# Kernel tuning notes

Measured on AMD Instinct MI355X. Metric: run time of the kernel, lower is better.

The kernel has to match this reference:

```python
import jax, jax.numpy as jnp
import numpy as np

N = 100000
E = 1600000

def gcn_conv(x, w, b, row, col, ew, n):
    # PyG GCNConv: linear transform, add self-loops (weight 1), symmetric
    # degree normalization with edge weights, scatter-sum to destinations.
    h = x @ w  # [N, out]
    loop = jnp.arange(n)
    row2 = jnp.concatenate([row, loop])
    col2 = jnp.concatenate([col, loop])
    ew2 = jnp.concatenate([ew, jnp.ones((n,), x.dtype)])
    deg = jax.ops.segment_sum(ew2, col2, num_segments=n)
    dinv = jnp.where(deg > 0, jax.lax.rsqrt(deg), jnp.zeros_like(deg))
    norm = dinv[row2] * ew2 * dinv[col2]  # [E+N]
    msg = h[row2] * norm[:, None]  # [E+N, out]
    out = jax.ops.segment_sum(msg, col2, num_segments=n)
    return out + b


def setup_inputs() -> dict:
    key = jax.random.key(0)
    ks = jax.random.split(key, 8)
    x = jax.random.normal(ks[0], (N, 256), dtype=jnp.float32)
    edge_index = jax.random.randint(ks[1], (2, E), 0, N, dtype=jnp.int64)
    edge_attr = jax.random.uniform(ks[2], (E,), dtype=jnp.float32)
    w_dense = jax.random.normal(ks[3], (256, 256), dtype=jnp.float32) * 0.05
    b_dense = jnp.zeros((256,), jnp.float32)
    w_enc = jax.random.normal(ks[4], (256, 256), dtype=jnp.float32) * 0.05
    b_enc = jnp.zeros((256,), jnp.float32)
    w_mu = jax.random.normal(ks[5], (256, 128), dtype=jnp.float32) * 0.05
    b_mu = jnp.zeros((128,), jnp.float32)
    w_logstd = jax.random.normal(ks[6], (256, 128), dtype=jnp.float32) * 0.05
    b_logstd = jnp.zeros((128,), jnp.float32)
    return {"x": x, "edge_index": edge_index, "edge_attr": edge_attr,
            "w_dense": w_dense, "b_dense": b_dense, "w_enc": w_enc, "b_enc": b_enc,
            "w_mu": w_mu, "b_mu": b_mu, "w_logstd": w_logstd, "b_logstd": b_logstd}


def reference(x, edge_index, edge_attr, w_dense, b_dense, w_enc, b_enc, w_mu, b_mu, w_logstd, b_logstd):
    row, col = edge_index[0], edge_index[1]
    h = jax.nn.relu(x @ w_dense + b_dense)  # dense + relu; dropout is identity in eval
    # enc_layer=2 -> encoder[:-1] applies exactly one hidden GCNConv
    h = gcn_conv(h, w_enc, b_enc, row, col, edge_attr, N)
    mu = gcn_conv(h, w_mu, b_mu, row, col, edge_attr, N)
    logstd = gcn_conv(h, w_logstd, b_logstd, row, col, edge_attr, N)
    return (mu, logstd)
```

## Files before the change

### kernel.cpp

```cpp
#include <hip/hip_runtime.h>


typedef short bf16x8 __attribute__((ext_vector_type(8)));
typedef float f32x4 __attribute__((ext_vector_type(4)));

static __device__ __forceinline__ unsigned int f2bf(float f) {
    unsigned int u = __float_as_uint(f);
    return ((u + 0x7fffu + ((u >> 16) & 1u)) >> 16) & 0xffffu;
}
static __device__ __forceinline__ float bf2f(unsigned int us) {
    return __uint_as_float(us << 16);
}

static __device__ __forceinline__ void load_lds16(const void* g, void* l) {
    __builtin_amdgcn_global_load_lds(
        (const __attribute__((address_space(1))) unsigned int*)g,
        (__attribute__((address_space(3))) unsigned int*)l, 16, 0, 0);
}

#define FIXSCALE 8388608.0f


__global__ __launch_bounds__(256) void init_kernel(unsigned long long* acc, int n) {
    int i = blockIdx.x * 256 + threadIdx.x;
    if (i < n) acc[i] = 0ull;
}

__global__ __launch_bounds__(256) void edge_pack_kernel(const int* __restrict__ col,
                                                        const float* __restrict__ ew,
                                                        unsigned long long* __restrict__ acc,
                                                        unsigned int* __restrict__ rank, int E) {
    int e = blockIdx.x * 256 + threadIdx.x;
    if (e < E) {
        int c = col[e];
        unsigned long long pk = (1ull << 32) |
                                (unsigned long long)(unsigned int)(ew[e] * FIXSCALE + 0.5f);
        unsigned long long old = atomicAdd(&acc[c], pk);
        rank[e] = (unsigned int)(old >> 32);
    }
}

__global__ __launch_bounds__(256) void dinv_kernel(const unsigned long long* __restrict__ acc,
                                                   float* __restrict__ dinv, int n) {
    int i = blockIdx.x * 256 + threadIdx.x;
    if (i < n) {
        float deg = 1.0f + (float)(unsigned int)acc[i] * (1.0f / FIXSCALE);
        dinv[i] = rsqrtf(deg);
    }
}

__global__ __launch_bounds__(1024) void scanA_kernel(const unsigned long long* __restrict__ acc,
                                                     int* __restrict__ offsets,
                                                     int* __restrict__ bsum, int n) {
    __shared__ int wsum[16];
    int tid = threadIdx.x, lane = tid & 63, wv = tid >> 6;
    int i = blockIdx.x * 1024 + tid;
    int v = (i < n) ? (int)(acc[i] >> 32) : 0;
    int s = v;
#pragma unroll
    for (int off = 1; off < 64; off <<= 1) {
        int t = __shfl_up(s, off, 64);
        if (lane >= off) s += t;
    }
    if (lane == 63) wsum[wv] = s;
    __syncthreads();
    if (wv == 0 && lane < 16) {
        int w = wsum[lane];
        int ss = w;
#pragma unroll
        for (int off = 1; off < 16; off <<= 1) {
            int t = __shfl_up(ss, off, 64);
            if (lane >= off) ss += t;
        }
        wsum[lane] = ss - w;
        if (lane == 15) bsum[blockIdx.x] = ss;
    }
    __syncthreads();
    if (i < n) offsets[i] = wsum[wv] + s - v;
}

__global__ __launch_bounds__(128) void scanB_kernel(int* __restrict__ bsum, int nb,
                                                    int* __restrict__ offsets, int n) {
    __shared__ int w0tot;
    int tid = threadIdx.x, lane = tid & 63, wv = tid >> 6;
    int v = (tid < nb) ? bsum[tid] : 0;
    int s = v;
#pragma unroll
    for (int off = 1; off < 64; off <<= 1) {
        int t = __shfl_up(s, off, 64);
        if (lane >= off) s += t;
    }
    if (wv == 0 && lane == 63) w0tot = s;
    __syncthreads();
    int excl = s - v + (wv ? w0tot : 0);
    if (tid < nb) bsum[tid] = excl;
    if (tid == nb - 1) offsets[n] = excl + v;
}

__global__ __launch_bounds__(256) void scanC_kernel(int* __restrict__ offsets,
                                                    const int* __restrict__ bsum, int n) {
    int i = blockIdx.x * 256 + threadIdx.x;
    if (i < n) offsets[i] += bsum[i >> 10];
}

__global__ __launch_bounds__(256) void fill2_kernel(const int* __restrict__ row,
                                                    const int* __restrict__ col,
                                                    const float* __restrict__ ew,
                                                    const unsigned int* __restrict__ rank,
                                                    const int* __restrict__ offsets,
                                                    const float* __restrict__ dinv,
                                                    uint2* __restrict__ edges, int E) {
    int e = blockIdx.x * 256 + threadIdx.x;
    if (e < E) {
        int c = col[e];
        int r = row[e];
        int pos = offsets[c] + (int)rank[e];
        uint2 p;
        p.x = (unsigned int)r;
        p.y = __float_as_uint(dinv[r] * ew[e]);
        edges[pos] = p;
    }
}

__global__ __launch_bounds__(256) void cvt_frag_kernel(const float* __restrict__ x,
                                                       unsigned short* __restrict__ Af, int n) {
    int g = blockIdx.x * 256 + threadIdx.x;
    int c = g >> 6, lane = g & 63;
    if (c >= n) return;
    float4 v = ((const float4*)x)[(size_t)c * 64 + lane];
    uint2 w;
    w.x = f2bf(v.x) | (f2bf(v.y) << 16);
    w.y = f2bf(v.z) | (f2bf(v.w) << 16);
    int T = c >> 4, l = c & 15;
    size_t idx8 = (size_t)T * 1024 + (size_t)((lane >> 3)) * 128 + ((lane >> 1) & 3) * 32 + l * 2 + (lane & 1);
    ((uint2*)Af)[idx8] = w;
}

__global__ __launch_bounds__(256) void splitw_kernel(const float* __restrict__ W, int M,
                                                     unsigned short* __restrict__ hi,
                                                     unsigned short* __restrict__ lo) {
    int idx = blockIdx.x * 256 + threadIdx.x;
    if (idx < M * 256) {
        int c = idx >> 8, k = idx & 255;
        float w = W[k * M + c];
        unsigned int h = f2bf(w);
        float r = w - bf2f(h);
        int T = c >> 4, l = c & 15, K = k >> 5, q = (k >> 3) & 3, j = k & 7;
        size_t o = (size_t)(T * 8 + K) * 512 + q * 128 + l * 8 + j;
        hi[o] = (unsigned short)h;
        lo[o] = (unsigned short)f2bf(r);
    }
}

__global__ __launch_bounds__(256) void bcat_kernel(const float* __restrict__ a,
                                                   const float* __restrict__ b,
                                                   float* __restrict__ o) {
    int t = threadIdx.x;
    o[t] = (t < 128) ? a[t] : b[t - 128];
}

#define ACC8(qv, uv)                                      \
    do {                                                  \
        float w_ = __uint_as_float((qv).y);               \
        a0 += w_ * __uint_as_float((uv).x << 16);         \
        a1 += w_ * __uint_as_float((uv).x & 0xffff0000u); \
        a2 += w_ * __uint_as_float((uv).y << 16);         \
        a3 += w_ * __uint_as_float((uv).y & 0xffff0000u); \
        a4 += w_ * __uint_as_float((uv).z << 16);         \
        a5 += w_ * __uint_as_float((uv).z & 0xffff0000u); \
        a6 += w_ * __uint_as_float((uv).w << 16);         \
        a7 += w_ * __uint_as_float((uv).w & 0xffff0000u); \
    } while (0)

__global__ __launch_bounds__(256) void spmm_kernel(const unsigned short* __restrict__ h,
                                                   const uint2* __restrict__ edges,
                                                   const int* __restrict__ offsets,
                                                   const float* __restrict__ dinv,
                                                   unsigned short* __restrict__ outf, int n) {
    int wave = threadIdx.x >> 6;
    int lane = threadIdx.x & 63;
    int half = lane >> 5, hl = lane & 31;
    int c = blockIdx.x * 4 + wave;
    if (c >= n) return;
    const uint4* __restrict__ h4 = (const uint4*)h;
    float di = dinv[c];
    int beg = __builtin_amdgcn_readfirstlane(offsets[c]);
    int end = __builtin_amdgcn_readfirstlane(offsets[c + 1]);
    int d = end - beg;
    int elim = beg + (d & ~1);

    float a0 = 0.f, a1 = 0.f, a2 = 0.f, a3 = 0.f;
    float a4 = 0.f, a5 = 0.f, a6 = 0.f, a7 = 0.f;

    int e = beg;
    for (; e + 8 <= elim; e += 8) {
        uint2 q0 = edges[e + 0 + half];
        uint2 q1 = edges[e + 2 + half];
        uint2 q2 = edges[e + 4 + half];
        uint2 q3 = edges[e + 6 + half];
        uint4 u0 = h4[(size_t)q0.x * 32 + hl];
        uint4 u1 = h4[(size_t)q1.x * 32 + hl];
        uint4 u2 = h4[(size_t)q2.x * 32 + hl];
        uint4 u3 = h4[(size_t)q3.x * 32 + hl];
        ACC8(q0, u0);
        ACC8(q1, u1);
        ACC8(q2, u2);
        ACC8(q3, u3);
    }
    for (; e < elim; e += 2) {
        uint2 q = edges[e + half];
        uint4 u = h4[(size_t)q.x * 32 + hl];
        ACC8(q, u);
    }
    {
        uint2 qf;
        qf.x = (unsigned int)c;
        qf.y = half ? 0u : __float_as_uint(di);
        if (half && (d & 1)) qf = edges[end - 1];
        uint4 uf = h4[(size_t)qf.x * 32 + hl];
        ACC8(qf, uf);
    }

    a0 += __shfl_xor(a0, 32);
    a1 += __shfl_xor(a1, 32);
    a2 += __shfl_xor(a2, 32);
    a3 += __shfl_xor(a3, 32);
    a4 += __shfl_xor(a4, 32);
    a5 += __shfl_xor(a5, 32);
    a6 += __shfl_xor(a6, 32);
    a7 += __shfl_xor(a7, 32);

    if (half == 0) {
        uint4 wv;
        wv.x = f2bf(di * a0) | (f2bf(di * a1) << 16);
        wv.y = f2bf(di * a2) | (f2bf(di * a3) << 16);
        wv.z = f2bf(di * a4) | (f2bf(di * a5) << 16);
        wv.w = f2bf(di * a6) | (f2bf(di * a7) << 16);
        int T = c >> 4, l = c & 15;
        size_t o16 = ((size_t)T * 8 + (hl >> 2)) * 512 + (size_t)(hl & 3) * 128 + (size_t)l * 8;
        *(uint4*)(outf + o16) = wv;
    }
}

__global__ __launch_bounds__(256) void mfma_gemm_kernel(const unsigned short* __restrict__ Af,
                                                        const unsigned short* __restrict__ Wh,
                                                        const unsigned short* __restrict__ Wl,
                                                        const float* __restrict__ bias,
                                                        void* __restrict__ outp,
                                                        int n, int M, int flags) {
    __shared__ short lds[12288];
    int tid = threadIdx.x, lane = tid & 63, wave = tid >> 6;
    int wr = wave & 1, wc = wave >> 1;
    int l16 = lane & 15, quad = lane >> 4;
    int T0 = blockIdx.x * 8;
    int Tc0 = blockIdx.y * 8;

    f32x4 acc[4][4];
#pragma unroll
    for (int i = 0; i < 4; ++i)
#pragma unroll
        for (int j = 0; j < 4; ++j) acc[i][j] = (f32x4)0.0f;

    for (int K = 0; K < 8; ++K) {
#pragma unroll
        for (int j = 0; j < 6; ++j) {
            int cid = wave * 6 + j;
            const unsigned short* g;
            if (cid < 8)       g = Af + ((size_t)(T0 + cid) * 8 + K) * 512;
            else if (cid < 16) g = Wh + ((size_t)(Tc0 + cid - 8) * 8 + K) * 512;
            else               g = Wl + ((size_t)(Tc0 + cid - 16) * 8 + K) * 512;
            load_lds16(g + (size_t)lane * 8, lds + cid * 512);
        }
        __syncthreads();
        bf16x8 af[4], bh[4], bl[4];
#pragma unroll
        for (int t = 0; t < 4; ++t) {
            af[t] = *(const bf16x8*)(lds + (4 * wr + t) * 512 + lane * 8);
            bh[t] = *(const bf16x8*)(lds + 4096 + (4 * wc + t) * 512 + lane * 8);
            bl[t] = *(const bf16x8*)(lds + 8192 + (4 * wc + t) * 512 + lane * 8);
        }
#pragma unroll
        for (int rt = 0; rt < 4; ++rt)
#pragma unroll
            for (int ct = 0; ct < 4; ++ct) {
                acc[rt][ct] = __builtin_amdgcn_mfma_f32_16x16x32_bf16(af[rt], bh[ct], acc[rt][ct], 0, 0, 0);
                acc[rt][ct] = __builtin_amdgcn_mfma_f32_16x16x32_bf16(af[rt], bl[ct], acc[rt][ct], 0, 0, 0);
            }
        __syncthreads();
    }

    int relu = flags & 1, obf = flags & 2, dual = flags & 4;
    int r0 = T0 * 16, c0 = Tc0 * 16;
#pragma unroll
    for (int ct = 0; ct < 4; ++ct) {
        int col = c0 + 64 * wc + 16 * ct + l16;
        float b = bias[col];
#pragma unroll
        for (int rt = 0; rt < 4; ++rt) {
            int rbase = r0 + 64 * wr + 16 * rt + quad * 4;
#pragma unroll
            for (int i = 0; i < 4; ++i) {
                int r = rbase + i;
                if (r < n) {
                    float v = acc[rt][ct][i] + b;
                    if (relu) v = fmaxf(v, 0.0f);
                    if (dual)
                        ((float*)outp)[(size_t)(col >> 7) * ((size_t)n * 128) + (size_t)r * 128 + (col & 127)] = v;
                    else if (obf)
                        ((unsigned short*)outp)[(size_t)r * M + col] = (unsigned short)f2bf(v);
                    else
                        ((float*)outp)[(size_t)r * M + col] = v;
                }
            }
        }
    }
}


extern "C" void kernel_launch(void* const* d_in, const int* in_sizes, int n_in,
                              void* d_out, int out_size, void* d_ws, size_t ws_size,
                              hipStream_t stream) {
    const float* x        = (const float*)d_in[0];
    const int*   ei       = (const int*)d_in[1];
    const float* ea       = (const float*)d_in[2];
    const float* w_dense  = (const float*)d_in[3];
    const float* b_dense  = (const float*)d_in[4];
    const float* w_enc    = (const float*)d_in[5];
    const float* b_enc    = (const float*)d_in[6];
    const float* w_mu     = (const float*)d_in[7];
    const float* b_mu     = (const float*)d_in[8];
    const float* w_logstd = (const float*)d_in[9];
    const float* b_logstd = (const float*)d_in[10];

    const int n = in_sizes[0] / 256;
    const int E = in_sizes[2];
    const int* row = ei;
    const int* col = ei + E;

    char* ws = (char*)d_ws;
    size_t off = 0;
    auto alloc = [&](size_t bytes) -> void* {
        void* p = ws + off;
        off = (off + bytes + 255) & ~(size_t)255;
        return p;
    };
    const int nTile = (n + 127) / 128;
    const int nTpad = nTile * 8;
    unsigned long long* acc = (unsigned long long*)alloc((size_t)n * 8);
    float* dinv   = (float*)alloc((size_t)n * 4);
    int*   offs   = (int*)alloc((size_t)(n + 1) * 4);
    int*   bsum   = (int*)alloc(128 * 4);
    unsigned int* rank = (unsigned int*)alloc((size_t)E * 4);
    uint2* edges  = (uint2*)alloc((size_t)E * 8);
    unsigned short* Af   = (unsigned short*)alloc((size_t)nTpad * 8192);
    unsigned short* wd_h = (unsigned short*)alloc(256 * 256 * 2);
    unsigned short* wd_l = (unsigned short*)alloc(256 * 256 * 2);
    unsigned short* we_h = (unsigned short*)alloc(256 * 256 * 2);
    unsigned short* we_l = (unsigned short*)alloc(256 * 256 * 2);
    unsigned short* wf_h = (unsigned short*)alloc(256 * 256 * 2);
    unsigned short* wf_l = (unsigned short*)alloc(256 * 256 * 2);
    float*          bcat = (float*)alloc(256 * 4);
    (void)ws_size;

    unsigned short* h1b = (unsigned short*)d_out;
    unsigned short* h0b = (unsigned short*)d_out + (size_t)n * 256;

    int nb_n = (n + 255) / 256;
    int nb_e = (E + 255) / 256;
    int nb_s = (n + 1023) / 1024;

    init_kernel<<<nb_n, 256, 0, stream>>>(acc, n);
    edge_pack_kernel<<<nb_e, 256, 0, stream>>>(col, ea, acc, rank, E);
    dinv_kernel<<<nb_n, 256, 0, stream>>>(acc, dinv, n);
    scanA_kernel<<<nb_s, 1024, 0, stream>>>(acc, offs, bsum, n);
    scanB_kernel<<<1, 128, 0, stream>>>(bsum, nb_s, offs, n);
    scanC_kernel<<<nb_n, 256, 0, stream>>>(offs, bsum, n);
    fill2_kernel<<<nb_e, 256, 0, stream>>>(row, col, ea, rank, offs, dinv, edges, E);

    cvt_frag_kernel<<<(n * 64 + 255) / 256, 256, 0, stream>>>(x, Af, n);
    splitw_kernel<<<256, 256, 0, stream>>>(w_dense, 256, wd_h, wd_l);
    splitw_kernel<<<256, 256, 0, stream>>>(w_enc, 256, we_h, we_l);
    splitw_kernel<<<128, 256, 0, stream>>>(w_mu, 128, wf_h, wf_l);
    splitw_kernel<<<128, 256, 0, stream>>>(w_logstd, 128, wf_h + 32768, wf_l + 32768);
    bcat_kernel<<<1, 256, 0, stream>>>(b_mu, b_logstd, bcat);

    mfma_gemm_kernel<<<dim3(nTile, 2), 256, 0, stream>>>(Af, wd_h, wd_l, b_dense, h0b, n, 256, 1 | 2);
    spmm_kernel<<<(n + 3) / 4, 256, 0, stream>>>(h0b, edges, offs, dinv, Af, n);
    mfma_gemm_kernel<<<dim3(nTile, 2), 256, 0, stream>>>(Af, we_h, we_l, b_enc, h1b, n, 256, 2);
    spmm_kernel<<<(n + 3) / 4, 256, 0, stream>>>(h1b, edges, offs, dinv, Af, n);
    mfma_gemm_kernel<<<dim3(nTile, 2), 256, 0, stream>>>(Af, wf_h, wf_l, bcat, d_out, n, 128, 4);
}
```

Before: 814.6 us.

## Privatize degree atomics into eight copies and split SpMM launches in halves

The per-destination 64-bit atomic counters are replicated eight ways, with the copy chosen by blockIdx&7, to reduce atomic contention in edge packing. A new kernel reduces the copies into counts and dinv, and another computes per-copy insertion offsets so the CSR fill stays stable. Each SpMM is also launched as two half-range kernels. This adds an 8x larger counter buffer, an extra pass over it, and more launches.

```diff
diff --git a/kernel.cpp b/kernel.cpp
--- a/kernel.cpp
+++ b/kernel.cpp
@@ -21,41 +21,52 @@
 #define FIXSCALE 8388608.0f
 
 
-__global__ __launch_bounds__(256) void init_kernel(unsigned long long* acc, int n) {
+__global__ __launch_bounds__(256) void init_kernel(unsigned long long* acc8, int n8) {
     int i = blockIdx.x * 256 + threadIdx.x;
-    if (i < n) acc[i] = 0ull;
+    if (i < n8) acc8[i] = 0ull;
 }
 
 __global__ __launch_bounds__(256) void edge_pack_kernel(const int* __restrict__ col,
                                                         const float* __restrict__ ew,
-                                                        unsigned long long* __restrict__ acc,
-                                                        unsigned int* __restrict__ rank, int E) {
+                                                        unsigned long long* __restrict__ acc8,
+                                                        unsigned int* __restrict__ rank,
+                                                        int E, int n) {
     int e = blockIdx.x * 256 + threadIdx.x;
     if (e < E) {
+        int p = blockIdx.x & 7;
         int c = col[e];
         unsigned long long pk = (1ull << 32) |
                                 (unsigned long long)(unsigned int)(ew[e] * FIXSCALE + 0.5f);
-        unsigned long long old = atomicAdd(&acc[c], pk);
+        unsigned long long old = atomicAdd(&acc8[(size_t)p * n + c], pk);
         rank[e] = (unsigned int)(old >> 32);
     }
 }
 
-__global__ __launch_bounds__(256) void dinv_kernel(const unsigned long long* __restrict__ acc,
-                                                   float* __restrict__ dinv, int n) {
+__global__ __launch_bounds__(256) void cnt_dinv_kernel(const unsigned long long* __restrict__ acc8,
+                                                       int* __restrict__ cnt,
+                                                       float* __restrict__ dinv, int n) {
     int i = blockIdx.x * 256 + threadIdx.x;
     if (i < n) {
-        float deg = 1.0f + (float)(unsigned int)acc[i] * (1.0f / FIXSCALE);
-        dinv[i] = rsqrtf(deg);
-    }
-}
-
-__global__ __launch_bounds__(1024) void scanA_kernel(const unsigned long long* __restrict__ acc,
+        int ct = 0;
+        unsigned long long ws = 0;
+#pragma unroll
+        for (int p = 0; p < 8; ++p) {
+            unsigned long long v = acc8[(size_t)p * n + i];
+            ct += (int)(v >> 32);
+            ws += (unsigned long long)(unsigned int)v;
+        }
+        cnt[i] = ct;
+        dinv[i] = rsqrtf(1.0f + (float)ws * (1.0f / FIXSCALE));
+    }
+}
+
+__global__ __launch_bounds__(1024) void scanA_kernel(const int* __restrict__ counts,
                                                      int* __restrict__ offsets,
                                                      int* __restrict__ bsum, int n) {
     __shared__ int wsum[16];
     int tid = threadIdx.x, lane = tid & 63, wv = tid >> 6;
     int i = blockIdx.x * 1024 + tid;
-    int v = (i < n) ? (int)(acc[i] >> 32) : 0;
+    int v = (i < n) ? counts[i] : 0;
     int s = v;
 #pragma unroll
     for (int off = 1; off < 64; off <<= 1) {
@@ -103,22 +114,37 @@
     if (i < n) offsets[i] += bsum[i >> 10];
 }
 
+__global__ __launch_bounds__(256) void copyoff_kernel(const unsigned long long* __restrict__ acc8,
+                                                      const int* __restrict__ offsets,
+                                                      int* __restrict__ copyOff, int n) {
+    int i = blockIdx.x * 256 + threadIdx.x;
+    if (i < n) {
+        int run = offsets[i];
+#pragma unroll
+        for (int p = 0; p < 8; ++p) {
+            copyOff[(size_t)p * n + i] = run;
+            run += (int)(acc8[(size_t)p * n + i] >> 32);
+        }
+    }
+}
+
 __global__ __launch_bounds__(256) void fill2_kernel(const int* __restrict__ row,
                                                     const int* __restrict__ col,
                                                     const float* __restrict__ ew,
                                                     const unsigned int* __restrict__ rank,
-                                                    const int* __restrict__ offsets,
+                                                    const int* __restrict__ copyOff,
                                                     const float* __restrict__ dinv,
-                                                    uint2* __restrict__ edges, int E) {
+                                                    uint2* __restrict__ edges, int E, int n) {
     int e = blockIdx.x * 256 + threadIdx.x;
     if (e < E) {
+        int p = blockIdx.x & 7;
         int c = col[e];
         int r = row[e];
-        int pos = offsets[c] + (int)rank[e];
-        uint2 p;
-        p.x = (unsigned int)r;
-        p.y = __float_as_uint(dinv[r] * ew[e]);
-        edges[pos] = p;
+        int pos = copyOff[(size_t)p * n + c] + (int)rank[e];
+        uint2 pk;
+        pk.x = (unsigned int)r;
+        pk.y = __float_as_uint(dinv[r] * ew[e]);
+        edges[pos] = pk;
     }
 }
 
@@ -176,11 +202,12 @@
                                                    const uint2* __restrict__ edges,
                                                    const int* __restrict__ offsets,
                                                    const float* __restrict__ dinv,
-                                                   unsigned short* __restrict__ outf, int n) {
+                                                   unsigned short* __restrict__ outf,
+                                                   int cbase, int n) {
     int wave = threadIdx.x >> 6;
     int lane = threadIdx.x & 63;
     int half = lane >> 5, hl = lane & 31;
-    int c = blockIdx.x * 4 + wave;
+    int c = cbase + blockIdx.x * 4 + wave;
     if (c >= n) return;
     const uint4* __restrict__ h4 = (const uint4*)h;
     float di = dinv[c];
@@ -346,10 +373,12 @@
     };
     const int nTile = (n + 127) / 128;
     const int nTpad = nTile * 8;
-    unsigned long long* acc = (unsigned long long*)alloc((size_t)n * 8);
+    unsigned long long* acc8 = (unsigned long long*)alloc((size_t)n * 8 * 8);
     float* dinv   = (float*)alloc((size_t)n * 4);
+    int*   cnt    = (int*)alloc((size_t)n * 4);
     int*   offs   = (int*)alloc((size_t)(n + 1) * 4);
     int*   bsum   = (int*)alloc(128 * 4);
+    int*   copyOff = (int*)alloc((size_t)n * 8 * 4);
     unsigned int* rank = (unsigned int*)alloc((size_t)E * 4);
     uint2* edges  = (uint2*)alloc((size_t)E * 8);
     unsigned short* Af   = (unsigned short*)alloc((size_t)nTpad * 8192);
@@ -368,14 +397,18 @@
     int nb_n = (n + 255) / 256;
     int nb_e = (E + 255) / 256;
     int nb_s = (n + 1023) / 1024;
-
-    init_kernel<<<nb_n, 256, 0, stream>>>(acc, n);
-    edge_pack_kernel<<<nb_e, 256, 0, stream>>>(col, ea, acc, rank, E);
-    dinv_kernel<<<nb_n, 256, 0, stream>>>(acc, dinv, n);
-    scanA_kernel<<<nb_s, 1024, 0, stream>>>(acc, offs, bsum, n);
+    int half1 = (n / 2) & ~3;
+    int nb_sp1 = (half1 + 3) / 4;
+    int nb_sp2 = (n - half1 + 3) / 4;
+
+    init_kernel<<<(n * 8 + 255) / 256, 256, 0, stream>>>(acc8, n * 8);
+    edge_pack_kernel<<<nb_e, 256, 0, stream>>>(col, ea, acc8, rank, E, n);
+    cnt_dinv_kernel<<<nb_n, 256, 0, stream>>>(acc8, cnt, dinv, n);
+    scanA_kernel<<<nb_s, 1024, 0, stream>>>(cnt, offs, bsum, n);
     scanB_kernel<<<1, 128, 0, stream>>>(bsum, nb_s, offs, n);
     scanC_kernel<<<nb_n, 256, 0, stream>>>(offs, bsum, n);
-    fill2_kernel<<<nb_e, 256, 0, stream>>>(row, col, ea, rank, offs, dinv, edges, E);
+    copyoff_kernel<<<nb_n, 256, 0, stream>>>(acc8, offs, copyOff, n);
+    fill2_kernel<<<nb_e, 256, 0, stream>>>(row, col, ea, rank, copyOff, dinv, edges, E, n);
 
     cvt_frag_kernel<<<(n * 64 + 255) / 256, 256, 0, stream>>>(x, Af, n);
     splitw_kernel<<<256, 256, 0, stream>>>(w_dense, 256, wd_h, wd_l);
@@ -385,8 +418,10 @@
     bcat_kernel<<<1, 256, 0, stream>>>(b_mu, b_logstd, bcat);
 
     mfma_gemm_kernel<<<dim3(nTile, 2), 256, 0, stream>>>(Af, wd_h, wd_l, b_dense, h0b, n, 256, 1 | 2);
-    spmm_kernel<<<(n + 3) / 4, 256, 0, stream>>>(h0b, edges, offs, dinv, Af, n);
+    spmm_kernel<<<nb_sp1, 256, 0, stream>>>(h0b, edges, offs, dinv, Af, 0, half1);
+    spmm_kernel<<<nb_sp2, 256, 0, stream>>>(h0b, edges, offs, dinv, Af, half1, n);
     mfma_gemm_kernel<<<dim3(nTile, 2), 256, 0, stream>>>(Af, we_h, we_l, b_enc, h1b, n, 256, 2);
-    spmm_kernel<<<(n + 3) / 4, 256, 0, stream>>>(h1b, edges, offs, dinv, Af, n);
+    spmm_kernel<<<nb_sp1, 256, 0, stream>>>(h1b, edges, offs, dinv, Af, 0, half1);
+    spmm_kernel<<<nb_sp2, 256, 0, stream>>>(h1b, edges, offs, dinv, Af, half1, n);
     mfma_gemm_kernel<<<dim3(nTile, 2), 256, 0, stream>>>(Af, wf_h, wf_l, bcat, d_out, n, 128, 4);
 }
```

New measurement: 832.6 us. 1.02x slower.
